# Performance work log

Hardware: AMD Instinct MI355X
Metric: run time of the kernel (lower is better)

## Reference

```python
import jax, jax.numpy as jnp
import numpy as np

V, E, H = 50000, 100, 128
B, S = 16, 4096
NUM_LEVELS = int(np.log2(S)) + 1  # 13; level l has S >> l nodes
# gate order in the 5-gate stack: i, f_l, f_r, o, u
XMAP = jnp.array([0, 1, 1, 2, 3])


def setup_inputs() -> dict:
    key = jax.random.key(0)
    ks = jax.random.split(key, 9)
    sE = 1.0 / np.sqrt(E)
    sH = 1.0 / np.sqrt(H)
    return {
        "embedding": jax.random.normal(ks[0], (V, E), jnp.float32) * 0.1,
        "W_x": jax.random.normal(ks[1], (4, H, E), jnp.float32) * sE,   # (i,f,o,u) x-projections
        "b_x": jax.random.normal(ks[2], (4, H), jnp.float32) * sE,
        "U_l": jax.random.normal(ks[3], (5, H, H), jnp.float32) * sH,   # (u_i_l,u_f_ll,u_f_rr,u_o_l,u_u_l) applied to h_left
        "b_l": jax.random.normal(ks[4], (5, H), jnp.float32) * sH,
        "U_r": jax.random.normal(ks[5], (5, H, H), jnp.float32) * sH,   # (u_i_r,u_f_lr,u_f_rl,u_o_r,u_u_r) applied to h_right
        "b_r": jax.random.normal(ks[6], (5, H), jnp.float32) * sH,
        "input_seq": jax.random.randint(ks[7], (B, S), 0, V, jnp.int32),
        "dep_tags": jax.random.randint(ks[8], (NUM_LEVELS - 1, S // 2), 0, S, jnp.int32),
    }


def _level_step(x5, h_l, h_r, c_l, c_r, U_l, b_l, U_r, b_r):
    # x5: [B,N,5,H] per-gate x contributions (w_*(x) incl. bias)
    pre = (x5
           + jnp.einsum('bnk,ghk->bngh', h_l, U_l) + b_l
           + jnp.einsum('bnk,ghk->bngh', h_r, U_r) + b_r)  # [B,N,5,H]
    i   = jax.nn.sigmoid(pre[:, :, 0])
    f_l = jax.nn.sigmoid(pre[:, :, 1])
    f_r = jax.nn.sigmoid(pre[:, :, 2])
    o   = jax.nn.sigmoid(pre[:, :, 3])
    u   = jnp.tanh(pre[:, :, 4])
    c = i * u + f_l * c_l + f_r * c_r
    h = o * jnp.tanh(c)
    return h, c


def reference(embedding, W_x, b_x, U_l, b_l, U_r, b_r, input_seq, dep_tags):
    b, s = input_seq.shape
    emb = embedding[input_seq]  # [B,S,E]
    xg = jnp.einsum('bse,ghe->bsgh', emb, W_x) + b_x  # [B,S,4,H]

    # level 0: every leaf is a token, children are zero
    z = jnp.zeros((b, s, xg.shape[-1]), xg.dtype)
    h, c = _level_step(xg[:, :, XMAP, :], z, z, z, z, U_l, b_l, U_r, b_r)

    for l in range(1, NUM_LEVELS):
        n = s >> l
        dep = dep_tags[l - 1, :n]                # token position re-embedded at each internal node
        x5 = xg[:, dep][:, :, XMAP, :]           # [B,N,5,H]
        hp = h.reshape(b, n, 2, -1)              # node i's children are (2i, 2i+1)
        cp = c.reshape(b, n, 2, -1)
        h, c = _level_step(x5, hp[:, :, 0], hp[:, :, 1], cp[:, :, 0], cp[:, :, 1],
                           U_l, b_l, U_r, b_r)
    return h[:, 0], c[:, 0]  # root (h, c): [B,H] each
```

## Files before the change

### kernel.cpp

```cpp
#include <hip/hip_runtime.h>
#include <hip/hip_bf16.h>

#define V_ 50000
#define E_ 100
#define H_ 128
#define B_ 16
#define S_ 4096

typedef unsigned short u16;
typedef unsigned int   u32;
typedef short bf16x8 __attribute__((ext_vector_type(8)));
typedef float f32x4  __attribute__((ext_vector_type(4)));

__device__ __forceinline__ float bf2f(u16 x) {
  return __uint_as_float(((u32)x) << 16);
}
__device__ __forceinline__ u16 f2bf(float x) {
  __hip_bfloat16 b = __float2bfloat16(x);
  return *reinterpret_cast<u16*>(&b);
}
__device__ __forceinline__ float sigm(float x) { return 1.0f / (1.0f + __expf(-x)); }
__device__ __forceinline__ float tanh_f(float x) {
  float e = __expf(2.0f * x);
  return 1.0f - 2.0f / (e + 1.0f);
}

#define PREP_N0 (V_ * 128)
#define PREP_N1 65536
#define PREP_N2 163840
#define PREP_N3 640
__global__ __launch_bounds__(256) void prep_all(
    const float* __restrict__ emb, const float* __restrict__ Wx,
    const float* __restrict__ Ul, const float* __restrict__ Ur,
    const float* __restrict__ bl, const float* __restrict__ br,
    u16* __restrict__ embB, u16* __restrict__ Bx, u16* __restrict__ Bu,
    float* __restrict__ bs)
{
  int i = blockIdx.x * 256 + threadIdx.x;
  if (i < PREP_N0) {
    int k = i & 127, t = i >> 7;
    embB[i] = (k < E_) ? f2bf(emb[t * E_ + k]) : (u16)0;
    return;
  }
  i -= PREP_N0;
  if (i < PREP_N1) {
    int j = i & 7, l = (i >> 3) & 63, s = (i >> 9) & 3, t = i >> 11;
    int k = s * 32 + (l >> 4) * 8 + j;
    int o = t * 16 + (l & 15);
    Bx[i] = (k < E_) ? f2bf(Wx[o * E_ + k]) : (u16)0;
    return;
  }
  i -= PREP_N1;
  if (i < PREP_N2) {
    int j = i & 7, l = (i >> 3) & 63, s = (i >> 9) & 7, t = i >> 12;
    int k = s * 32 + (l >> 4) * 8 + j;
    int gh = t * 16 + (l & 15);
    float v = (k < 128) ? Ul[gh * 128 + k] : Ur[gh * 128 + (k - 128)];
    Bu[i] = f2bf(v);
    return;
  }
  i -= PREP_N2;
  if (i < PREP_N3) bs[i] = bl[i] + br[i];
}

#define XLDS 516
__global__ __launch_bounds__(512) void xg_mfma(
    const u16* __restrict__ embB, const u16* __restrict__ Bx,
    const float* __restrict__ bx, const int* __restrict__ seq,
    const float* __restrict__ bs,
    ushort4* __restrict__ xg, u16* __restrict__ h0, float* __restrict__ c0)
{
  __shared__ u16 lds[32 * XLDS];
  const int w = threadIdx.x >> 6, lane = threadIdx.x & 63;
  const int quad = lane >> 4, l15 = lane & 15;
  const int m0 = blockIdx.x * 32;

  f32x4 acc[2][4];
  #pragma unroll
  for (int r = 0; r < 2; ++r)
    #pragma unroll
    for (int t = 0; t < 4; ++t) acc[r][t] = (f32x4){0.f, 0.f, 0.f, 0.f};

  int tok0 = seq[m0 + l15];
  int tok1 = seq[m0 + 16 + l15];
  const u16* a0p = embB + (size_t)tok0 * 128 + quad * 8;
  const u16* a1p = embB + (size_t)tok1 * 128 + quad * 8;

  #pragma unroll
  for (int s = 0; s < 4; ++s) {
    bf16x8 a0 = *reinterpret_cast<const bf16x8*>(a0p + s * 32);
    bf16x8 a1 = *reinterpret_cast<const bf16x8*>(a1p + s * 32);
    #pragma unroll
    for (int ti = 0; ti < 4; ++ti) {
      int t = w * 4 + ti;
      bf16x8 b = *reinterpret_cast<const bf16x8*>(Bx + ((size_t)(t * 4 + s) * 64 + lane) * 8);
      acc[0][ti] = __builtin_amdgcn_mfma_f32_16x16x32_bf16(a0, b, acc[0][ti], 0, 0, 0);
      acc[1][ti] = __builtin_amdgcn_mfma_f32_16x16x32_bf16(a1, b, acc[1][ti], 0, 0, 0);
    }
  }

  const int g = w >> 1;
  #pragma unroll
  for (int ti = 0; ti < 4; ++ti) {
    int o = (w * 4 + ti) * 16 + l15;
    float bxo = bx[o];
    int hhw = (w & 1) * 64 + ti * 16 + l15;
    #pragma unroll
    for (int r = 0; r < 2; ++r)
      #pragma unroll
      for (int reg = 0; reg < 4; ++reg) {
        int mrow = r * 16 + quad * 4 + reg;
        lds[mrow * XLDS + hhw * 4 + g] = f2bf(acc[r][ti][reg] + bxo);
      }
  }
  __syncthreads();

  #pragma unroll
  for (int i = 0; i < 8; ++i) {
    int pidx = i * 512 + threadIdx.x;
    int m = pidx >> 7, hh = pidx & 127;
    ushort4 v = *reinterpret_cast<const ushort4*>(&lds[m * XLDS + hh * 4]);
    size_t gm = (size_t)(m0 + m);
    xg[gm * 128 + hh] = v;
    float pi = bf2f(v.x) + bs[hh];
    float po = bf2f(v.z) + bs[384 + hh];
    float pu = bf2f(v.w) + bs[512 + hh];
    float c = sigm(pi) * tanh_f(pu);
    float h = sigm(po) * tanh_f(c);
    h0[gm * 128 + hh] = f2bf(h);
    c0[gm * 128 + hh] = c;
  }
}

__global__ __launch_bounds__(512) void level_mfma(
    const ushort4* __restrict__ xg4, const int* __restrict__ deprow,
    const u16* __restrict__ Bu, const float* __restrict__ bs,
    const u16* __restrict__ hPrev, const float* __restrict__ cPrev,
    u16* __restrict__ hOut, float* __restrict__ cOut, int n, int ln2n)
{
  const int w = threadIdx.x >> 6, lane = threadIdx.x & 63;
  const int quad = lane >> 4, l15 = lane & 15;
  const int hh = w * 16 + l15;
  const int m0 = blockIdx.x * 32;

  ushort4 xv[8];
  float clv[8], crv[8];
  #pragma unroll
  for (int i = 0; i < 8; ++i) {
    int m = m0 + (i >> 2) * 16 + quad * 4 + (i & 3);
    int j = m & (n - 1);
    int b = m >> ln2n;
    int dj = deprow[j];
    xv[i] = xg4[((size_t)b * S_ + dj) * 128 + hh];
    clv[i] = cPrev[(size_t)m * 256 + hh];
    crv[i] = cPrev[(size_t)m * 256 + 128 + hh];
  }

  f32x4 acc[2][5];
  #pragma unroll
  for (int r = 0; r < 2; ++r)
    #pragma unroll
    for (int g = 0; g < 5; ++g) acc[r][g] = (f32x4){0.f, 0.f, 0.f, 0.f};

  const u16* a0p = hPrev + (size_t)(m0 + l15) * 256 + quad * 8;
  const u16* a1p = a0p + 16 * 256;

  #pragma unroll
  for (int s = 0; s < 8; ++s) {
    bf16x8 a0 = *reinterpret_cast<const bf16x8*>(a0p + s * 32);
    bf16x8 a1 = *reinterpret_cast<const bf16x8*>(a1p + s * 32);
    #pragma unroll
    for (int g = 0; g < 5; ++g) {
      int t = g * 8 + w;
      bf16x8 b = *reinterpret_cast<const bf16x8*>(Bu + ((size_t)(t * 8 + s) * 64 + lane) * 8);
      acc[0][g] = __builtin_amdgcn_mfma_f32_16x16x32_bf16(a0, b, acc[0][g], 0, 0, 0);
      acc[1][g] = __builtin_amdgcn_mfma_f32_16x16x32_bf16(a1, b, acc[1][g], 0, 0, 0);
    }
  }

  float bsv[5];
  #pragma unroll
  for (int g = 0; g < 5; ++g) bsv[g] = bs[g * 128 + hh];

  #pragma unroll
  for (int i = 0; i < 8; ++i) {
    int r = i >> 2, reg = i & 3;
    int m = m0 + r * 16 + quad * 4 + reg;
    ushort4 v = xv[i];
    float x0 = bf2f(v.x), x1 = bf2f(v.y), x2 = bf2f(v.z), x3 = bf2f(v.w);
    float pi  = acc[r][0][reg] + x0 + bsv[0];
    float pfl = acc[r][1][reg] + x1 + bsv[1];
    float pfr = acc[r][2][reg] + x1 + bsv[2];
    float po  = acc[r][3][reg] + x2 + bsv[3];
    float pu  = acc[r][4][reg] + x3 + bsv[4];
    float c = sigm(pi) * tanh_f(pu) + sigm(pfl) * clv[i] + sigm(pfr) * crv[i];
    float h = sigm(po) * tanh_f(c);
    hOut[(size_t)m * 128 + hh] = f2bf(h);
    cOut[(size_t)m * 128 + hh] = c;
  }
}

template<int LVL>
__device__ __forceinline__ void deep_step(
    const ushort4* __restrict__ xg4, const int* __restrict__ dep,
    const u16* __restrict__ Bu, const float* __restrict__ bsv,
    const u16* __restrict__ h6, const float* __restrict__ c6,
    const u16* __restrict__ hsrc, const float* __restrict__ csrc,
    u16* __restrict__ hdst, float* __restrict__ cdst,
    int b, int w, int lane, int quad, int l15, int hh,
    float* __restrict__ out)
{
  constexpr int nb = 4096 >> LVL;
  constexpr int nr = (LVL == 7) ? 2 : 1;

  ushort4 xv[nr][4];
  float clv[nr][4], crv[nr][4];
  #pragma unroll
  for (int r = 0; r < nr; ++r)
    #pragma unroll
    for (int reg = 0; reg < 4; ++reg) {
      int j = r * 16 + quad * 4 + reg;
      if (j < nb) {
        int dj = dep[(LVL - 1) * (S_ / 2) + j];
        xv[r][reg] = xg4[((size_t)b * S_ + dj) * 128 + hh];
        if constexpr (LVL == 7) {
          clv[r][reg] = c6[(size_t)(b * 32 + j) * 256 + hh];
          crv[r][reg] = c6[(size_t)(b * 32 + j) * 256 + 128 + hh];
        } else {
          clv[r][reg] = csrc[(2 * j) * 128 + hh];
          crv[r][reg] = csrc[(2 * j + 1) * 128 + hh];
        }
      }
    }

  f32x4 acc[nr][5];
  #pragma unroll
  for (int r = 0; r < nr; ++r)
    #pragma unroll
    for (int g = 0; g < 5; ++g) acc[r][g] = (f32x4){0.f, 0.f, 0.f, 0.f};

  #pragma unroll
  for (int s = 0; s < 8; ++s) {
    bf16x8 a[nr];
    if constexpr (LVL == 7) {
      const u16* ap = h6 + (size_t)(b * 32 + l15) * 256 + s * 32 + quad * 8;
      a[0] = *reinterpret_cast<const bf16x8*>(ap);
      a[1] = *reinterpret_cast<const bf16x8*>(ap + 16 * 256);
    } else {
      int child = 2 * l15 + (s >= 4 ? 1 : 0);
      int kk = (s & 3) * 32 + quad * 8;
      a[0] = *reinterpret_cast<const bf16x8*>(&hsrc[child * 136 + kk]);
    }
    #pragma unroll
    for (int g = 0; g < 5; ++g) {
      int t = g * 8 + w;
      bf16x8 bb = *reinterpret_cast<const bf16x8*>(Bu + ((size_t)(t * 8 + s) * 64 + lane) * 8);
      #pragma unroll
      for (int r = 0; r < nr; ++r)
        acc[r][g] = __builtin_amdgcn_mfma_f32_16x16x32_bf16(a[r], bb, acc[r][g], 0, 0, 0);
    }
  }

  #pragma unroll
  for (int r = 0; r < nr; ++r)
    #pragma unroll
    for (int reg = 0; reg < 4; ++reg) {
      int j = r * 16 + quad * 4 + reg;
      if (j < nb) {
        ushort4 v = xv[r][reg];
        float x0 = bf2f(v.x), x1 = bf2f(v.y), x2 = bf2f(v.z), x3 = bf2f(v.w);
        float pi  = acc[r][0][reg] + x0 + bsv[0];
        float pfl = acc[r][1][reg] + x1 + bsv[1];
        float pfr = acc[r][2][reg] + x1 + bsv[2];
        float po  = acc[r][3][reg] + x2 + bsv[3];
        float pu  = acc[r][4][reg] + x3 + bsv[4];
        float c = sigm(pi) * tanh_f(pu) + sigm(pfl) * clv[r][reg] + sigm(pfr) * crv[r][reg];
        float h = sigm(po) * tanh_f(c);
        hdst[j * 136 + hh] = f2bf(h);
        cdst[j * 128 + hh] = c;
        if constexpr (LVL == 12) {
          out[b * 128 + hh] = h;
          out[2048 + b * 128 + hh] = c;
        }
      }
    }
}

__global__ __launch_bounds__(512) void deep_fused(
    const ushort4* __restrict__ xg4, const int* __restrict__ dep,
    const u16* __restrict__ Bu, const float* __restrict__ bs,
    const u16* __restrict__ h6, const float* __restrict__ c6,
    float* __restrict__ out)
{
  __shared__ u16  hls[2][32 * 136];
  __shared__ float cls[2][32 * 128];
  const int b = blockIdx.x;
  const int w = threadIdx.x >> 6, lane = threadIdx.x & 63;
  const int quad = lane >> 4, l15 = lane & 15;
  const int hh = w * 16 + l15;

  float bsv[5];
  #pragma unroll
  for (int g = 0; g < 5; ++g) bsv[g] = bs[g * 128 + hh];

  deep_step<7>(xg4, dep, Bu, bsv, h6, c6, hls[1], cls[1], hls[0], cls[0],
               b, w, lane, quad, l15, hh, out);
  __syncthreads();
  deep_step<8>(xg4, dep, Bu, bsv, h6, c6, hls[0], cls[0], hls[1], cls[1],
               b, w, lane, quad, l15, hh, out);
  __syncthreads();
  deep_step<9>(xg4, dep, Bu, bsv, h6, c6, hls[1], cls[1], hls[0], cls[0],
               b, w, lane, quad, l15, hh, out);
  __syncthreads();
  deep_step<10>(xg4, dep, Bu, bsv, h6, c6, hls[0], cls[0], hls[1], cls[1],
                b, w, lane, quad, l15, hh, out);
  __syncthreads();
  deep_step<11>(xg4, dep, Bu, bsv, h6, c6, hls[1], cls[1], hls[0], cls[0],
                b, w, lane, quad, l15, hh, out);
  __syncthreads();
  deep_step<12>(xg4, dep, Bu, bsv, h6, c6, hls[0], cls[0], hls[1], cls[1],
                b, w, lane, quad, l15, hh, out);
}

extern "C" void kernel_launch(void* const* d_in, const int* in_sizes, int n_in,
                              void* d_out, int out_size, void* d_ws, size_t ws_size,
                              hipStream_t stream)
{
  const float* emb = (const float*)d_in[0];
  const float* Wx  = (const float*)d_in[1];
  const float* bx  = (const float*)d_in[2];
  const float* Ul  = (const float*)d_in[3];
  const float* bl  = (const float*)d_in[4];
  const float* Ur  = (const float*)d_in[5];
  const float* br  = (const float*)d_in[6];
  const int* seq = (const int*)d_in[7];
  const int* dep = (const int*)d_in[8];

  char* p = (char*)d_ws;
  u16* embB = (u16*)p;   p += (size_t)V_ * 128 * 2;
  u16* BswX = (u16*)p;   p += 131072;
  u16* BswU = (u16*)p;   p += 327680;
  float* bs = (float*)p; p += 4096;
  u16* xg = (u16*)p;     p += (size_t)B_ * S_ * 512 * 2;
  u16* hA = (u16*)p;     p += (size_t)B_ * S_ * H_ * 2;
  float* cA = (float*)p; p += (size_t)B_ * S_ * H_ * 4;
  u16* hB = (u16*)p;     p += (size_t)B_ * (S_ / 2) * H_ * 2;
  float* cB = (float*)p; p += (size_t)B_ * (S_ / 2) * H_ * 4;

  const int prep_tot = PREP_N0 + PREP_N1 + PREP_N2 + PREP_N3;
  prep_all<<<dim3((prep_tot + 255) / 256), dim3(256), 0, stream>>>(
      emb, Wx, Ul, Ur, bl, br, embB, BswX, BswU, bs);

  xg_mfma<<<dim3(B_ * S_ / 32), dim3(512), 0, stream>>>(
      embB, BswX, bx, seq, bs, (ushort4*)xg, hA, cA);

  const ushort4* xg4 = (const ushort4*)xg;
  u16 *hp = hA, *ho = hB;
  float *cp = cA, *co = cB;
  for (int l = 1; l <= 6; ++l) {
    int n = S_ >> l;
    int Mtot = B_ * n;
    const int* deprow = dep + (size_t)(l - 1) * (S_ / 2);
    level_mfma<<<dim3(Mtot / 32), dim3(512), 0, stream>>>(
        xg4, deprow, BswU, bs, hp, cp, ho, co, n, 12 - l);
    u16* th = hp; hp = ho; ho = th;
    float* tc = cp; cp = co; co = tc;
  }

  deep_fused<<<dim3(16), dim3(512), 0, stream>>>(
      xg4, dep, BswU, bs, hp, cp, (float*)d_out);
}
```

Measured before the change: 275.9 us.

## Run levels 7-8 as grid kernels and fuse only levels 9-12

Result: slower. 294.5 us (+6.7%).

```diff
diff --git a/kernel.cpp b/kernel.cpp
--- a/kernel.cpp
+++ b/kernel.cpp
@@ -201,95 +201,75 @@
 }
 
 template<int LVL>
-__device__ __forceinline__ void deep_step(
-    const ushort4* __restrict__ xg4, const int* __restrict__ dep,
+__device__ __forceinline__ void deep94_step(
     const u16* __restrict__ Bu, const float* __restrict__ bsv,
-    const u16* __restrict__ h6, const float* __restrict__ c6,
+    const bf16x8* __restrict__ a9,
+    const float* __restrict__ cl9, const float* __restrict__ cr9,
+    const ushort4* __restrict__ xv,
     const u16* __restrict__ hsrc, const float* __restrict__ csrc,
     u16* __restrict__ hdst, float* __restrict__ cdst,
     int b, int w, int lane, int quad, int l15, int hh,
     float* __restrict__ out)
 {
   constexpr int nb = 4096 >> LVL;
-  constexpr int nr = (LVL == 7) ? 2 : 1;
-
-  ushort4 xv[nr][4];
-  float clv[nr][4], crv[nr][4];
-  #pragma unroll
-  for (int r = 0; r < nr; ++r)
-    #pragma unroll
-    for (int reg = 0; reg < 4; ++reg) {
-      int j = r * 16 + quad * 4 + reg;
-      if (j < nb) {
-        int dj = dep[(LVL - 1) * (S_ / 2) + j];
-        xv[r][reg] = xg4[((size_t)b * S_ + dj) * 128 + hh];
-        if constexpr (LVL == 7) {
-          clv[r][reg] = c6[(size_t)(b * 32 + j) * 256 + hh];
-          crv[r][reg] = c6[(size_t)(b * 32 + j) * 256 + 128 + hh];
-        } else {
-          clv[r][reg] = csrc[(2 * j) * 128 + hh];
-          crv[r][reg] = csrc[(2 * j + 1) * 128 + hh];
-        }
-      }
-    }
-
-  f32x4 acc[nr][5];
-  #pragma unroll
-  for (int r = 0; r < nr; ++r)
-    #pragma unroll
-    for (int g = 0; g < 5; ++g) acc[r][g] = (f32x4){0.f, 0.f, 0.f, 0.f};
+
+  f32x4 acc[5];
+  #pragma unroll
+  for (int g = 0; g < 5; ++g) acc[g] = (f32x4){0.f, 0.f, 0.f, 0.f};
 
   #pragma unroll
   for (int s = 0; s < 8; ++s) {
-    bf16x8 a[nr];
-    if constexpr (LVL == 7) {
-      const u16* ap = h6 + (size_t)(b * 32 + l15) * 256 + s * 32 + quad * 8;
-      a[0] = *reinterpret_cast<const bf16x8*>(ap);
-      a[1] = *reinterpret_cast<const bf16x8*>(ap + 16 * 256);
+    bf16x8 a;
+    if constexpr (LVL == 9) {
+      a = a9[s];
     } else {
       int child = 2 * l15 + (s >= 4 ? 1 : 0);
       int kk = (s & 3) * 32 + quad * 8;
-      a[0] = *reinterpret_cast<const bf16x8*>(&hsrc[child * 136 + kk]);
+      a = *reinterpret_cast<const bf16x8*>(&hsrc[child * 136 + kk]);
     }
     #pragma unroll
     for (int g = 0; g < 5; ++g) {
       int t = g * 8 + w;
       bf16x8 bb = *reinterpret_cast<const bf16x8*>(Bu + ((size_t)(t * 8 + s) * 64 + lane) * 8);
-      #pragma unroll
-      for (int r = 0; r < nr; ++r)
-        acc[r][g] = __builtin_amdgcn_mfma_f32_16x16x32_bf16(a[r], bb, acc[r][g], 0, 0, 0);
-    }
-  }
-
-  #pragma unroll
-  for (int r = 0; r < nr; ++r)
-    #pragma unroll
-    for (int reg = 0; reg < 4; ++reg) {
-      int j = r * 16 + quad * 4 + reg;
-      if (j < nb) {
-        ushort4 v = xv[r][reg];
-        float x0 = bf2f(v.x), x1 = bf2f(v.y), x2 = bf2f(v.z), x3 = bf2f(v.w);
-        float pi  = acc[r][0][reg] + x0 + bsv[0];
-        float pfl = acc[r][1][reg] + x1 + bsv[1];
-        float pfr = acc[r][2][reg] + x1 + bsv[2];
-        float po  = acc[r][3][reg] + x2 + bsv[3];
-        float pu  = acc[r][4][reg] + x3 + bsv[4];
-        float c = sigm(pi) * tanh_f(pu) + sigm(pfl) * clv[r][reg] + sigm(pfr) * crv[r][reg];
-        float h = sigm(po) * tanh_f(c);
-        hdst[j * 136 + hh] = f2bf(h);
-        cdst[j * 128 + hh] = c;
-        if constexpr (LVL == 12) {
-          out[b * 128 + hh] = h;
-          out[2048 + b * 128 + hh] = c;
-        }
+      acc[g] = __builtin_amdgcn_mfma_f32_16x16x32_bf16(a, bb, acc[g], 0, 0, 0);
+    }
+  }
+
+  #pragma unroll
+  for (int reg = 0; reg < 4; ++reg) {
+    int j = quad * 4 + reg;
+    if (j < nb) {
+      ushort4 v = xv[reg];
+      float x0 = bf2f(v.x), x1 = bf2f(v.y), x2 = bf2f(v.z), x3 = bf2f(v.w);
+      float cl, cr;
+      if constexpr (LVL == 9) {
+        cl = cl9[reg];
+        cr = cr9[reg];
+      } else {
+        cl = csrc[(2 * j) * 128 + hh];
+        cr = csrc[(2 * j + 1) * 128 + hh];
       }
-    }
-}
-
-__global__ __launch_bounds__(512) void deep_fused(
+      float pi  = acc[0][reg] + x0 + bsv[0];
+      float pfl = acc[1][reg] + x1 + bsv[1];
+      float pfr = acc[2][reg] + x1 + bsv[2];
+      float po  = acc[3][reg] + x2 + bsv[3];
+      float pu  = acc[4][reg] + x3 + bsv[4];
+      float c = sigm(pi) * tanh_f(pu) + sigm(pfl) * cl + sigm(pfr) * cr;
+      float h = sigm(po) * tanh_f(c);
+      hdst[j * 136 + hh] = f2bf(h);
+      cdst[j * 128 + hh] = c;
+      if constexpr (LVL == 12) {
+        out[b * 128 + hh] = h;
+        out[2048 + b * 128 + hh] = c;
+      }
+    }
+  }
+}
+
+__global__ __launch_bounds__(512) void deep_fused94(
     const ushort4* __restrict__ xg4, const int* __restrict__ dep,
     const u16* __restrict__ Bu, const float* __restrict__ bs,
-    const u16* __restrict__ h6, const float* __restrict__ c6,
+    const u16* __restrict__ h8, const float* __restrict__ c8,
     float* __restrict__ out)
 {
   __shared__ u16  hls[2][32 * 136];
@@ -299,27 +279,47 @@
   const int quad = lane >> 4, l15 = lane & 15;
   const int hh = w * 16 + l15;
 
+  bf16x8 a9[8];
+  #pragma unroll
+  for (int s = 0; s < 8; ++s)
+    a9[s] = *reinterpret_cast<const bf16x8*>(
+        h8 + (size_t)(b * 8 + l15) * 256 + s * 32 + quad * 8);
+
+  float cl9[4], cr9[4];
+  #pragma unroll
+  for (int reg = 0; reg < 4; ++reg) {
+    int j = quad * 4 + reg;
+    if (j < 8) {
+      cl9[reg] = c8[(size_t)(b * 8 + j) * 256 + hh];
+      cr9[reg] = c8[(size_t)(b * 8 + j) * 256 + 128 + hh];
+    }
+  }
+
+  ushort4 xv9[4], xv10[4], xv11[4], xv12[4];
+  #pragma unroll
+  for (int reg = 0; reg < 4; ++reg) {
+    int j = quad * 4 + reg;
+    if (j < 8)  xv9[reg]  = xg4[((size_t)b * S_ + dep[8  * 2048 + j]) * 128 + hh];
+    if (j < 4)  xv10[reg] = xg4[((size_t)b * S_ + dep[9  * 2048 + j]) * 128 + hh];
+    if (j < 2)  xv11[reg] = xg4[((size_t)b * S_ + dep[10 * 2048 + j]) * 128 + hh];
+    if (j < 1)  xv12[reg] = xg4[((size_t)b * S_ + dep[11 * 2048 + j]) * 128 + hh];
+  }
+
   float bsv[5];
   #pragma unroll
   for (int g = 0; g < 5; ++g) bsv[g] = bs[g * 128 + hh];
 
-  deep_step<7>(xg4, dep, Bu, bsv, h6, c6, hls[1], cls[1], hls[0], cls[0],
-               b, w, lane, quad, l15, hh, out);
+  deep94_step<9>(Bu, bsv, a9, cl9, cr9, xv9, hls[1], cls[1], hls[0], cls[0],
+                 b, w, lane, quad, l15, hh, out);
   __syncthreads();
-  deep_step<8>(xg4, dep, Bu, bsv, h6, c6, hls[0], cls[0], hls[1], cls[1],
-               b, w, lane, quad, l15, hh, out);
+  deep94_step<10>(Bu, bsv, a9, cl9, cr9, xv10, hls[0], cls[0], hls[1], cls[1],
+                  b, w, lane, quad, l15, hh, out);
   __syncthreads();
-  deep_step<9>(xg4, dep, Bu, bsv, h6, c6, hls[1], cls[1], hls[0], cls[0],
-               b, w, lane, quad, l15, hh, out);
+  deep94_step<11>(Bu, bsv, a9, cl9, cr9, xv11, hls[1], cls[1], hls[0], cls[0],
+                  b, w, lane, quad, l15, hh, out);
   __syncthreads();
-  deep_step<10>(xg4, dep, Bu, bsv, h6, c6, hls[0], cls[0], hls[1], cls[1],
-                b, w, lane, quad, l15, hh, out);
-  __syncthreads();
-  deep_step<11>(xg4, dep, Bu, bsv, h6, c6, hls[1], cls[1], hls[0], cls[0],
-                b, w, lane, quad, l15, hh, out);
-  __syncthreads();
-  deep_step<12>(xg4, dep, Bu, bsv, h6, c6, hls[0], cls[0], hls[1], cls[1],
-                b, w, lane, quad, l15, hh, out);
+  deep94_step<12>(Bu, bsv, a9, cl9, cr9, xv12, hls[0], cls[0], hls[1], cls[1],
+                  b, w, lane, quad, l15, hh, out);
 }
 
 extern "C" void kernel_launch(void* const* d_in, const int* in_sizes, int n_in,
@@ -357,7 +357,7 @@
   const ushort4* xg4 = (const ushort4*)xg;
   u16 *hp = hA, *ho = hB;
   float *cp = cA, *co = cB;
-  for (int l = 1; l <= 6; ++l) {
+  for (int l = 1; l <= 8; ++l) {
     int n = S_ >> l;
     int Mtot = B_ * n;
     const int* deprow = dep + (size_t)(l - 1) * (S_ / 2);
@@ -367,6 +367,6 @@
     float* tc = cp; cp = co; co = tc;
   }
 
-  deep_fused<<<dim3(16), dim3(512), 0, stream>>>(
+  deep_fused94<<<dim3(16), dim3(512), 0, stream>>>(
       xg4, dep, BswU, bs, hp, cp, (float*)d_out);
 }
```
